# Optimization experiments

Hardware: AMD Instinct MI355X
Metric: run time of the kernel (lower is better)

The kernel has to match this reference:

```python
import jax, jax.numpy as jnp
from jax import lax
import numpy as np

B, T, H, K = 128, 256, 768, 64


def setup_inputs() -> dict:
    key = jax.random.key(0)
    k1, k2, k3, k4 = jax.random.split(key, 4)
    hidden = jax.random.normal(k1, (B, T, H), dtype=jnp.float32)
    masks = jnp.ones((B, T), dtype=jnp.int32)
    target = jax.random.randint(k2, (B, T), 0, K, dtype=jnp.int32)
    W = jax.random.normal(k3, (H, K), dtype=jnp.float32) * 0.02
    b = jnp.zeros((K,), dtype=jnp.float32)
    transitions = jax.random.uniform(k4, (K, K), dtype=jnp.float32)
    return {"hidden": hidden, "masks": masks, "target": target,
            "W": W, "b": b, "transitions": transitions}


def _crf_log_norm(emissions, trans, seq_len):
    # emissions: [B,T,K]; forward algorithm (log-sum-exp recurrence over time)
    Tn = emissions.shape[1]
    alpha0 = emissions[:, 0]  # [B,K]

    def step(alpha, xs):
        emis_t, t = xs
        new = jax.nn.logsumexp(alpha[:, :, None] + trans[None], axis=1) + emis_t
        alpha = jnp.where((t < seq_len)[:, None], new, alpha)
        return alpha, None

    xs = (jnp.swapaxes(emissions[:, 1:], 0, 1), jnp.arange(1, Tn))
    alpha, _ = lax.scan(step, alpha0, xs)
    return jax.nn.logsumexp(alpha, axis=1)  # [B]


def _crf_sequence_score(emissions, tags, trans, seq_len):
    Tn = emissions.shape[1]
    t_idx = jnp.arange(Tn)
    valid = t_idx[None, :] < seq_len[:, None]  # [B,T]
    unary = jnp.take_along_axis(emissions, tags[..., None], axis=2)[..., 0]
    unary = jnp.sum(jnp.where(valid, unary, 0.0), axis=1)
    pair = trans[tags[:, :-1], tags[:, 1:]]  # [B,T-1]
    valid_pair = t_idx[1:][None, :] < seq_len[:, None]
    binary = jnp.sum(jnp.where(valid_pair, pair, 0.0), axis=1)
    return unary + binary


def _crf_decode(emissions, trans, seq_len):
    # Viterbi with backpointers; padded steps carry state (identity backptr)
    Bn, Tn, Kn = emissions.shape
    v0 = emissions[:, 0]

    def step(v, xs):
        emis_t, t = xs
        scores = v[:, :, None] + trans[None]  # [B, K_prev, K_cur]
        bp = jnp.argmax(scores, axis=1).astype(jnp.int32)
        new_v = jnp.max(scores, axis=1) + emis_t
        m = (t < seq_len)[:, None]
        v = jnp.where(m, new_v, v)
        bp = jnp.where(m, bp, jnp.arange(Kn, dtype=jnp.int32)[None])
        return v, bp

    xs = (jnp.swapaxes(emissions[:, 1:], 0, 1), jnp.arange(1, Tn))
    v, bps = lax.scan(step, v0, xs)  # bps: [T-1, B, K]
    best_score = jnp.max(v, axis=1)
    last_tag = jnp.argmax(v, axis=1).astype(jnp.int32)

    def back(tag, bp_t):
        prev = jnp.take_along_axis(bp_t, tag[:, None], axis=1)[:, 0]
        return prev, prev

    _, rev_tags = lax.scan(back, last_tag, bps, reverse=True)  # [T-1, B]
    path = jnp.concatenate([rev_tags, last_tag[None]], axis=0)  # [T, B]
    path = jnp.swapaxes(path, 0, 1)  # [B, T]
    valid = jnp.arange(Tn)[None, :] < seq_len[:, None]
    path = jnp.where(valid, path, 0)
    return path, best_score


def reference(hidden, masks, target, W, b, transitions):
    # dense projection (dropout omitted for determinism)
    emissions = jnp.einsum('bth,hk->btk', hidden, W) + b  # [B,T,K]
    seq_len = jnp.sum(masks, axis=1).astype(jnp.int32)
    log_norm = _crf_log_norm(emissions, transitions, seq_len)
    seq_score = _crf_sequence_score(emissions, target, transitions, seq_len)
    log_likelihood = seq_score - log_norm  # [B]
    decode_predict, _crf_scores = _crf_decode(emissions, transitions, seq_len)
    return decode_predict, log_likelihood
```

## Files before the change

kernel.cpp:

```cpp
#include <hip/hip_runtime.h>

#define B_ 128
#define T_ 256
#define H_ 768
#define K_ 64
#define BT_ (B_ * T_)

template <int CTRL>
__device__ __forceinline__ float dpp_mov_f(float x) {
    return __int_as_float(__builtin_amdgcn_update_dpp(
        __float_as_int(x), __float_as_int(x), CTRL, 0xF, 0xF, false));
}
__device__ __forceinline__ float wave_max64(float x) {
    x = fmaxf(x, dpp_mov_f<0x111>(x));
    x = fmaxf(x, dpp_mov_f<0x112>(x));
    x = fmaxf(x, dpp_mov_f<0x114>(x));
    x = fmaxf(x, dpp_mov_f<0x118>(x));
    x = fmaxf(x, dpp_mov_f<0x142>(x));
    x = fmaxf(x, dpp_mov_f<0x143>(x));
    return __int_as_float(__builtin_amdgcn_readlane(__float_as_int(x), 63));
}
__device__ __forceinline__ float readlane0_f(float x) {
    return __int_as_float(__builtin_amdgcn_readfirstlane(__float_as_int(x)));
}

#define BK_ 32
#define P_ 130
__global__ __launch_bounds__(256) void gemm_emis(const float* __restrict__ hidden,
                                                 const float* __restrict__ W,
                                                 const float* __restrict__ bias,
                                                 float* __restrict__ emis) {
    __shared__ float At[BK_ * P_];

    const int tid = threadIdx.x;
    const int lane = tid & 63;
    const int wc = __builtin_amdgcn_readfirstlane((tid >> 6) * 16);
    const int rowbase = blockIdx.x * 128;

    const int srow = tid >> 3;
    const int sh4 = tid & 7;

    float acc0[16], acc1[16];
#pragma unroll
    for (int c = 0; c < 16; ++c) { acc0[c] = bias[wc + c]; acc1[c] = acc0[c]; }

    float4 pf[4];
#pragma unroll
    for (int i = 0; i < 4; ++i)
        pf[i] = *(const float4*)&hidden[(rowbase + srow + i * 32) * H_ + sh4 * 4];

    for (int kb = 0; kb < H_ / BK_; ++kb) {
        __syncthreads();
#pragma unroll
        for (int i = 0; i < 4; ++i) {
            int row = srow + i * 32;
            At[(sh4 * 4 + 0) * P_ + row] = pf[i].x;
            At[(sh4 * 4 + 1) * P_ + row] = pf[i].y;
            At[(sh4 * 4 + 2) * P_ + row] = pf[i].z;
            At[(sh4 * 4 + 3) * P_ + row] = pf[i].w;
        }
        __syncthreads();
        if (kb + 1 < H_ / BK_) {
#pragma unroll
            for (int i = 0; i < 4; ++i)
                pf[i] = *(const float4*)&hidden[(rowbase + srow + i * 32) * H_ +
                                                (kb + 1) * BK_ + sh4 * 4];
        }
        const float* Wk = &W[(kb * BK_) * K_ + wc];
#pragma unroll 8
        for (int h = 0; h < BK_; ++h) {
            float2 a = *(const float2*)&At[h * P_ + 2 * lane];
            float4 w0 = *(const float4*)&Wk[h * K_ + 0];
            float4 w1 = *(const float4*)&Wk[h * K_ + 4];
            float4 w2 = *(const float4*)&Wk[h * K_ + 8];
            float4 w3 = *(const float4*)&Wk[h * K_ + 12];
            acc0[0]  += a.x * w0.x; acc1[0]  += a.y * w0.x;
            acc0[1]  += a.x * w0.y; acc1[1]  += a.y * w0.y;
            acc0[2]  += a.x * w0.z; acc1[2]  += a.y * w0.z;
            acc0[3]  += a.x * w0.w; acc1[3]  += a.y * w0.w;
            acc0[4]  += a.x * w1.x; acc1[4]  += a.y * w1.x;
            acc0[5]  += a.x * w1.y; acc1[5]  += a.y * w1.y;
            acc0[6]  += a.x * w1.z; acc1[6]  += a.y * w1.z;
            acc0[7]  += a.x * w1.w; acc1[7]  += a.y * w1.w;
            acc0[8]  += a.x * w2.x; acc1[8]  += a.y * w2.x;
            acc0[9]  += a.x * w2.y; acc1[9]  += a.y * w2.y;
            acc0[10] += a.x * w2.z; acc1[10] += a.y * w2.z;
            acc0[11] += a.x * w2.w; acc1[11] += a.y * w2.w;
            acc0[12] += a.x * w3.x; acc1[12] += a.y * w3.x;
            acc0[13] += a.x * w3.y; acc1[13] += a.y * w3.y;
            acc0[14] += a.x * w3.z; acc1[14] += a.y * w3.z;
            acc0[15] += a.x * w3.w; acc1[15] += a.y * w3.w;
        }
    }

    float* e0 = &emis[(size_t)(rowbase + 2 * lane) * K_ + wc];
    float* e1 = &emis[(size_t)(rowbase + 2 * lane + 1) * K_ + wc];
#pragma unroll
    for (int q = 0; q < 4; ++q) {
        *(float4*)&e0[q * 4] = make_float4(acc0[q * 4], acc0[q * 4 + 1],
                                           acc0[q * 4 + 2], acc0[q * 4 + 3]);
        *(float4*)&e1[q * 4] = make_float4(acc1[q * 4], acc1[q * 4 + 1],
                                           acc1[q * 4 + 2], acc1[q * 4 + 3]);
    }
}

__global__ __launch_bounds__(64, 1) void crf_kernel(const float* __restrict__ emis,
                                                    const int* __restrict__ masks,
                                                    const int* __restrict__ target,
                                                    const float* __restrict__ trans,
                                                    float* __restrict__ out) {
    __shared__ __align__(16) float vbuf[T_ * K_];
    __shared__ float tbuf[K_ * 65];

    const int lane = threadIdx.x;
    const int bid = blockIdx.x;
    const int b = (bid < B_) ? bid : bid - B_;

    int sl = 0;
#pragma unroll
    for (int k = 0; k < 4; ++k) sl += masks[b * T_ + lane + k * 64];
#pragma unroll
    for (int m = 32; m; m >>= 1) sl += __shfl_xor(sl, m, 64);
    const int seq_len = sl;

    const float* eb = emis + (size_t)b * (T_ * K_);

    if (bid < B_) {
        float Ecol[64];
#pragma unroll
        for (int i = 0; i < 64; ++i) Ecol[i] = __expf(trans[i * K_ + lane]);

        float e0 = eb[lane];
        float a00 = readlane0_f(e0);
        float r = __expf(e0 - a00);
        float c = a00;

        float e_cur = eb[K_ + lane];
        float e0_cur = readlane0_f(e_cur);
        float x_cur = __expf(e_cur - e0_cur);

        for (int t = 1; t < T_; ++t) {
            float e_nxt = (t < T_ - 1) ? eb[(t + 1) * K_ + lane] : 0.f;
            vbuf[lane] = r;
            float s0 = 0.f, s1 = 0.f, s2 = 0.f, s3 = 0.f;
#pragma unroll
            for (int i = 0; i < 16; ++i) {
                float4 p4 = *(const float4*)&vbuf[i * 4];
                s0 += p4.x * Ecol[i * 4 + 0];
                s1 += p4.y * Ecol[i * 4 + 1];
                s2 += p4.z * Ecol[i * 4 + 2];
                s3 += p4.w * Ecol[i * 4 + 3];
            }
            float S = (s0 + s1) + (s2 + s3);
            float S0 = readlane0_f(S);
            if (t < seq_len) {
                r = __fdividef(S * x_cur, S0);
                c += __logf(S0) + e0_cur;
            }
            e_cur = e_nxt;
            e0_cur = readlane0_f(e_cur);
            x_cur = __expf(e_cur - e0_cur);
        }
        float rs = r;
#pragma unroll
        for (int m = 32; m; m >>= 1) rs += __shfl_xor(rs, m, 64);
        float log_norm = c + __logf(rs);

        float sc = 0.f;
#pragma unroll
        for (int k = 0; k < 4; ++k) {
            int t = lane + k * 64;
            if (t < seq_len) {
                int tg = target[b * T_ + t];
                sc += eb[t * K_ + tg];
                if (t >= 1) sc += trans[target[b * T_ + t - 1] * K_ + tg];
            }
        }
#pragma unroll
        for (int m = 32; m; m >>= 1) sc += __shfl_xor(sc, m, 64);
        if (lane == 0) out[BT_ + b] = sc - log_norm;
    } else {
        float Tcol[64];
#pragma unroll
        for (int i = 0; i < 64; ++i) Tcol[i] = trans[i * K_ + lane];
        for (int idx = lane; idx < K_ * K_; idx += 64)
            tbuf[(idx >> 6) * 65 + (idx & 63)] = trans[idx];

        float v = eb[lane];
        vbuf[lane] = v;
        float e_cur = eb[K_ + lane];
        for (int t = 1; t < T_; ++t) {
            float e_nxt = (t < T_ - 1) ? eb[(t + 1) * K_ + lane] : 0.f;
            const float* vp = &vbuf[(t - 1) * K_];
            float mm[4];
            mm[0] = mm[1] = mm[2] = mm[3] = -3.4e38f;
#pragma unroll
            for (int i = 0; i < 16; ++i) {
                float4 v4 = *(const float4*)&vp[i * 4];
                float q = fmaxf(fmaxf(v4.x + Tcol[i * 4 + 0], v4.y + Tcol[i * 4 + 1]),
                                fmaxf(v4.z + Tcol[i * 4 + 2], v4.w + Tcol[i * 4 + 3]));
                mm[i & 3] = fmaxf(mm[i & 3], q);
            }
            float M = fmaxf(fmaxf(mm[0], mm[1]), fmaxf(mm[2], mm[3]));
            if (t < seq_len) v = M + e_cur;
            vbuf[t * K_ + lane] = v;
            e_cur = e_nxt;
        }

        float M = wave_max64(v);
        unsigned long long ball = __ballot(v >= M);
        int tag = (int)__builtin_ctzll(ball);

        int path[4];
#pragma unroll
        for (int k = 0; k < 4; ++k) path[k] = 0;
        if (lane == ((T_ - 1) & 63)) path[(T_ - 1) >> 6] = tag;

        float vpre = vbuf[(T_ - 2) * K_ + lane];
        for (int t = T_ - 1; t >= 1; --t) {
            float vnext = (t >= 2) ? vbuf[(t - 2) * K_ + lane] : 0.f;
            if (t < seq_len) {
                float s = vpre + tbuf[lane * 65 + tag];
                float Ms = wave_max64(s);
                unsigned long long bl = __ballot(s >= Ms);
                tag = (int)__builtin_ctzll(bl);
            }
            int p = t - 1;
            if (lane == (p & 63)) path[p >> 6] = tag;
            vpre = vnext;
        }
#pragma unroll
        for (int k = 0; k < 4; ++k) {
            int t = lane + k * 64;
            out[b * T_ + t] = (t < seq_len) ? (float)path[k] : 0.f;
        }
    }
}

extern "C" void kernel_launch(void* const* d_in, const int* in_sizes, int n_in,
                              void* d_out, int out_size, void* d_ws, size_t ws_size,
                              hipStream_t stream) {
    const float* hidden = (const float*)d_in[0];
    const int* masks    = (const int*)d_in[1];
    const int* target   = (const int*)d_in[2];
    const float* W      = (const float*)d_in[3];
    const float* bias   = (const float*)d_in[4];
    const float* trans  = (const float*)d_in[5];
    float* out = (float*)d_out;
    float* emis = (float*)d_ws;

    gemm_emis<<<dim3(BT_ / 128), dim3(256), 0, stream>>>(hidden, W, bias, emis);
    crf_kernel<<<dim3(2 * B_), dim3(64), 0, stream>>>(emis, masks, target, trans, out);
}
```

Before: 390.8 us.

## Merge forward and Viterbi waves into one block with emissions staged in LDS

The CRF kernel now runs one 128-thread block per sequence. Wave 0 does the forward algorithm and wave 1 does Viterbi, where before they were separate 64-thread blocks. Each block first copies the sequence's emissions into shared memory so the serial recurrences read from LDS instead of global memory. The forward step is also restructured: the normalisation reciprocal and log for the next step are computed off the critical path, and both inner loops load all operands before reducing into 8 accumulators for more ILP. The costs are a large LDS footprint (about 2x64KB plus extras), which may exceed limits or reduce occupancy, and half as many blocks across the GPU.

Measured after the change: 387.5 us. About the same (-0.8%).

```diff
diff --git a/kernel.cpp b/kernel.cpp
--- a/kernel.cpp
+++ b/kernel.cpp
@@ -36,7 +36,6 @@
     const int lane = tid & 63;
     const int wc = __builtin_amdgcn_readfirstlane((tid >> 6) * 16);
     const int rowbase = blockIdx.x * 128;
-
     const int srow = tid >> 3;
     const int sh4 = tid & 7;
 
@@ -104,67 +103,83 @@
     }
 }
 
-__global__ __launch_bounds__(64, 1) void crf_kernel(const float* __restrict__ emis,
-                                                    const int* __restrict__ masks,
-                                                    const int* __restrict__ target,
-                                                    const float* __restrict__ trans,
-                                                    float* __restrict__ out) {
+__global__ __launch_bounds__(128, 1) void crf_kernel(const float* __restrict__ emis,
+                                                     const int* __restrict__ masks,
+                                                     const int* __restrict__ target,
+                                                     const float* __restrict__ trans,
+                                                     float* __restrict__ out) {
+    __shared__ __align__(16) float ebuf[T_ * K_];
     __shared__ __align__(16) float vbuf[T_ * K_];
     __shared__ float tbuf[K_ * 65];
-
-    const int lane = threadIdx.x;
-    const int bid = blockIdx.x;
-    const int b = (bid < B_) ? bid : bid - B_;
-
+    __shared__ __align__(16) float pbuf[64];
+
+    const int tid = threadIdx.x;
+    const int lane = tid & 63;
+    const int b = blockIdx.x;
+    const float* eb = emis + (size_t)b * (T_ * K_);
+
+    {
+        const float4* src = (const float4*)eb;
+        float4* dst = (float4*)ebuf;
+#pragma unroll
+        for (int k = 0; k < 32; ++k) dst[tid + k * 128] = src[tid + k * 128];
+    }
     int sl = 0;
 #pragma unroll
     for (int k = 0; k < 4; ++k) sl += masks[b * T_ + lane + k * 64];
 #pragma unroll
     for (int m = 32; m; m >>= 1) sl += __shfl_xor(sl, m, 64);
     const int seq_len = sl;
-
-    const float* eb = emis + (size_t)b * (T_ * K_);
-
-    if (bid < B_) {
+    __syncthreads();
+
+    if (tid < 64) {
         float Ecol[64];
 #pragma unroll
         for (int i = 0; i < 64; ++i) Ecol[i] = __expf(trans[i * K_ + lane]);
 
-        float e0 = eb[lane];
-        float a00 = readlane0_f(e0);
-        float r = __expf(e0 - a00);
-        float c = a00;
-
-        float e_cur = eb[K_ + lane];
-        float e0_cur = readlane0_f(e_cur);
-        float x_cur = __expf(e_cur - e0_cur);
+        float e_c = ebuf[lane];
+        float e00 = readlane0_f(e_c);
+        float p = __expf(e_c - e00);
+        float C = e00;
+        float logD0prev = 0.f;
+        float e_n = ebuf[K_ + lane];
+        float en0 = readlane0_f(e_n);
+        float xg = __expf(e_n - en0);
 
         for (int t = 1; t < T_; ++t) {
-            float e_nxt = (t < T_ - 1) ? eb[(t + 1) * K_ + lane] : 0.f;
-            vbuf[lane] = r;
-            float s0 = 0.f, s1 = 0.f, s2 = 0.f, s3 = 0.f;
-#pragma unroll
-            for (int i = 0; i < 16; ++i) {
-                float4 p4 = *(const float4*)&vbuf[i * 4];
-                s0 += p4.x * Ecol[i * 4 + 0];
-                s1 += p4.y * Ecol[i * 4 + 1];
-                s2 += p4.z * Ecol[i * 4 + 2];
-                s3 += p4.w * Ecol[i * 4 + 3];
-            }
-            float S = (s0 + s1) + (s2 + s3);
-            float S0 = readlane0_f(S);
-            if (t < seq_len) {
-                r = __fdividef(S * x_cur, S0);
-                c += __logf(S0) + e0_cur;
-            }
-            e_cur = e_nxt;
-            e0_cur = readlane0_f(e_cur);
-            x_cur = __expf(e_cur - e0_cur);
-        }
-        float rs = r;
+            pbuf[lane] = p;
+            float e_f = (t < T_ - 1) ? ebuf[(t + 1) * K_ + lane] : 0.f;
+            float4 q[16];
+#pragma unroll
+            for (int i = 0; i < 16; ++i) q[i] = ((const float4*)pbuf)[i];
+            float a0 = 0.f, a1 = 0.f, a2 = 0.f, a3 = 0.f;
+            float a4 = 0.f, a5 = 0.f, a6 = 0.f, a7 = 0.f;
+#pragma unroll
+            for (int i = 0; i < 8; ++i) {
+                a0 += q[2 * i].x     * Ecol[8 * i + 0];
+                a1 += q[2 * i].y     * Ecol[8 * i + 1];
+                a2 += q[2 * i].z     * Ecol[8 * i + 2];
+                a3 += q[2 * i].w     * Ecol[8 * i + 3];
+                a4 += q[2 * i + 1].x * Ecol[8 * i + 4];
+                a5 += q[2 * i + 1].y * Ecol[8 * i + 5];
+                a6 += q[2 * i + 1].z * Ecol[8 * i + 6];
+                a7 += q[2 * i + 1].w * Ecol[8 * i + 7];
+            }
+            float D = ((a0 + a1) + (a2 + a3)) + ((a4 + a5) + (a6 + a7));
+            float pnew = D * xg;
+            bool run = (t < seq_len);
+            if (run) { p = pnew; C += en0 + logD0prev; }
+            float D0 = readlane0_f(D);
+            logD0prev = __logf(D0);
+            float gn = __fdividef(1.f, D0);
+            en0 = readlane0_f(e_f);
+            xg = __expf(e_f - en0) * gn;
+            e_n = e_f;
+        }
+        float rs = p;
 #pragma unroll
         for (int m = 32; m; m >>= 1) rs += __shfl_xor(rs, m, 64);
-        float log_norm = c + __logf(rs);
+        float log_norm = C + __logf(rs);
 
         float sc = 0.f;
 #pragma unroll
@@ -172,7 +187,7 @@
             int t = lane + k * 64;
             if (t < seq_len) {
                 int tg = target[b * T_ + t];
-                sc += eb[t * K_ + tg];
+                sc += ebuf[t * K_ + tg];
                 if (t >= 1) sc += trans[target[b * T_ + t - 1] * K_ + tg];
             }
         }
@@ -186,25 +201,34 @@
         for (int idx = lane; idx < K_ * K_; idx += 64)
             tbuf[(idx >> 6) * 65 + (idx & 63)] = trans[idx];
 
-        float v = eb[lane];
+        float v = ebuf[lane];
         vbuf[lane] = v;
-        float e_cur = eb[K_ + lane];
+        float e_n = ebuf[K_ + lane];
         for (int t = 1; t < T_; ++t) {
-            float e_nxt = (t < T_ - 1) ? eb[(t + 1) * K_ + lane] : 0.f;
-            const float* vp = &vbuf[(t - 1) * K_];
-            float mm[4];
-            mm[0] = mm[1] = mm[2] = mm[3] = -3.4e38f;
-#pragma unroll
-            for (int i = 0; i < 16; ++i) {
-                float4 v4 = *(const float4*)&vp[i * 4];
-                float q = fmaxf(fmaxf(v4.x + Tcol[i * 4 + 0], v4.y + Tcol[i * 4 + 1]),
-                                fmaxf(v4.z + Tcol[i * 4 + 2], v4.w + Tcol[i * 4 + 3]));
-                mm[i & 3] = fmaxf(mm[i & 3], q);
-            }
-            float M = fmaxf(fmaxf(mm[0], mm[1]), fmaxf(mm[2], mm[3]));
-            if (t < seq_len) v = M + e_cur;
+            float e_f = (t < T_ - 1) ? ebuf[(t + 1) * K_ + lane] : 0.f;
+            float4 q[16];
+            const float4* vp = (const float4*)&vbuf[(t - 1) * K_];
+#pragma unroll
+            for (int i = 0; i < 16; ++i) q[i] = vp[i];
+            float m0 = -3.4e38f, m1 = m0, m2 = m0, m3 = m0;
+            float m4 = m0, m5 = m0, m6 = m0, m7 = m0;
+#pragma unroll
+            for (int i = 0; i < 8; ++i) {
+                m0 = fmaxf(m0, q[2 * i].x     + Tcol[8 * i + 0]);
+                m1 = fmaxf(m1, q[2 * i].y     + Tcol[8 * i + 1]);
+                m2 = fmaxf(m2, q[2 * i].z     + Tcol[8 * i + 2]);
+                m3 = fmaxf(m3, q[2 * i].w     + Tcol[8 * i + 3]);
+                m4 = fmaxf(m4, q[2 * i + 1].x + Tcol[8 * i + 4]);
+                m5 = fmaxf(m5, q[2 * i + 1].y + Tcol[8 * i + 5]);
+                m6 = fmaxf(m6, q[2 * i + 1].z + Tcol[8 * i + 6]);
+                m7 = fmaxf(m7, q[2 * i + 1].w + Tcol[8 * i + 7]);
+            }
+            float M = fmaxf(fmaxf(fmaxf(m0, m1), fmaxf(m2, m3)),
+                            fmaxf(fmaxf(m4, m5), fmaxf(m6, m7)));
+            float vn = M + e_n;
+            if (t < seq_len) v = vn;
             vbuf[t * K_ + lane] = v;
-            e_cur = e_nxt;
+            e_n = e_f;
         }
 
         float M = wave_max64(v);
@@ -225,8 +249,8 @@
                 unsigned long long bl = __ballot(s >= Ms);
                 tag = (int)__builtin_ctzll(bl);
             }
-            int p = t - 1;
-            if (lane == (p & 63)) path[p >> 6] = tag;
+            int pidx = t - 1;
+            if (lane == (pidx & 63)) path[pidx >> 6] = tag;
             vpre = vnext;
         }
 #pragma unroll
@@ -250,5 +274,5 @@
     float* emis = (float*)d_ws;
 
     gemm_emis<<<dim3(BT_ / 128), dim3(256), 0, stream>>>(hidden, W, bias, emis);
-    crf_kernel<<<dim3(2 * B_), dim3(64), 0, stream>>>(emis, masks, target, trans, out);
-}
+    crf_kernel<<<dim3(B_), dim3(128), 0, stream>>>(emis, masks, target, trans, out);
+}
```
